# Kernel optimization log

Measured on AMD Instinct MI355X. Metric: run time of the kernel, lower is better.

The kernel has to match this reference:

```python
import jax, jax.numpy as jnp
import numpy as np

N_NODES = 50000
N_EDGES = 1600000
D_FEAT = 48


def setup_inputs() -> dict:
    key = jax.random.key(0)
    k1, k2, k3, k4, k5 = jax.random.split(key, 5)
    return {
        "x": jax.random.normal(k1, (N_EDGES, D_FEAT), dtype=jnp.float32),
        "switch": jax.random.uniform(k2, (N_EDGES,), dtype=jnp.float32),
        "edge_src": jax.random.randint(k3, (N_EDGES,), 0, N_NODES, dtype=jnp.int32),
        "edge_dst": jax.random.randint(k4, (N_EDGES,), 0, N_NODES, dtype=jnp.int32),
        "species": jax.random.randint(k5, (N_NODES,), 0, 100, dtype=jnp.int32),
    }


def reference(x, switch, edge_src, edge_dst, species):
    # nat = number of atoms, taken from species shape (static)
    nat = species.shape[0]
    # apply_switch: multiply per-edge switch into edge features [E, D] * [E, 1]
    xw = x * switch[:, None]
    # scatter-add edges to source atoms
    out = jax.ops.segment_sum(xw, edge_src, num_segments=nat)
    # antisymmetric: subtract scatter-add to destination atoms
    out = out - jax.ops.segment_sum(xw, edge_dst, num_segments=nat)
    return out  # [nat, D]
```

## Files before the change

### kernel.cpp

```cpp
#include <hip/hip_runtime.h>
#include <hip/hip_bf16.h>
#include <hip/hip_fp16.h>
#include <math.h>


#define D_FEAT 48
#define RNODES 64
#define RSHIFT 6
#define NB_MAX 1024
#define EPB 4096
#define SORT_CAP 8192

__global__ __launch_bounds__(256) void convert_kernel(
        const float4* __restrict__ x4, const float* __restrict__ sw,
        uint4* __restrict__ xwh, int G) {
    int g = blockIdx.x * 256 + threadIdx.x;
    if (g >= G) return;
    unsigned ug = (unsigned)g;
    int e = (int)(ug / 6u);
    float s = sw[e];
    const float4* p = x4 + (size_t)g * 2;
    float4 a = p[0], b = p[1];
    __half2 h0 = __floats2half2_rn(a.x * s, a.y * s);
    __half2 h1 = __floats2half2_rn(a.z * s, a.w * s);
    __half2 h2 = __floats2half2_rn(b.x * s, b.y * s);
    __half2 h3 = __floats2half2_rn(b.z * s, b.w * s);
    uint4 o;
    o.x = __builtin_bit_cast(unsigned int, h0);
    o.y = __builtin_bit_cast(unsigned int, h1);
    o.z = __builtin_bit_cast(unsigned int, h2);
    o.w = __builtin_bit_cast(unsigned int, h3);
    xwh[g] = o;
}

__global__ __launch_bounds__(256) void hist_kernel(
        const int* __restrict__ src, const int* __restrict__ dst,
        int* __restrict__ gcnt, int E, int NB) {
    __shared__ int lh[NB_MAX];
    for (int b = threadIdx.x; b < NB; b += 256) lh[b] = 0;
    __syncthreads();
    int t = threadIdx.x;
    int base = blockIdx.x * EPB;
    #pragma unroll
    for (int i = 0; i < EPB / 1024; ++i) {
        int e = base + i * 1024 + t * 4;
        if (e + 3 < E) {
            int4 s4 = *(const int4*)(src + e);
            int4 d4 = *(const int4*)(dst + e);
            atomicAdd(&lh[s4.x >> RSHIFT], 1);
            atomicAdd(&lh[s4.y >> RSHIFT], 1);
            atomicAdd(&lh[s4.z >> RSHIFT], 1);
            atomicAdd(&lh[s4.w >> RSHIFT], 1);
            atomicAdd(&lh[d4.x >> RSHIFT], 1);
            atomicAdd(&lh[d4.y >> RSHIFT], 1);
            atomicAdd(&lh[d4.z >> RSHIFT], 1);
            atomicAdd(&lh[d4.w >> RSHIFT], 1);
        } else {
            for (int j = 0; j < 4; ++j) {
                int ee = e + j;
                if (ee < E) {
                    atomicAdd(&lh[src[ee] >> RSHIFT], 1);
                    atomicAdd(&lh[dst[ee] >> RSHIFT], 1);
                }
            }
        }
    }
    __syncthreads();
    for (int b = threadIdx.x; b < NB; b += 256) {
        int c = lh[b];
        if (c) atomicAdd(&gcnt[b], c);
    }
}

__global__ __launch_bounds__(1024) void scan_kernel(
        const int* __restrict__ gcnt, int* __restrict__ goff,
        int* __restrict__ gcur, int* __restrict__ noff,
        int NB, int N, int total) {
    __shared__ int s[NB_MAX];
    int t = threadIdx.x;
    int v = (t < NB) ? gcnt[t] : 0;
    s[t] = v;
    __syncthreads();
    for (int d = 1; d < 1024; d <<= 1) {
        int a = (t >= d) ? s[t - d] : 0;
        __syncthreads();
        s[t] += a;
        __syncthreads();
    }
    if (t < NB) {
        int excl = s[t] - v;
        goff[t] = excl;
        gcur[t] = excl;
    }
    if (t == 0) {
        goff[NB] = total;
        noff[N] = total;
    }
}

__device__ __forceinline__ void bin_place(int e, int node, int side,
                                          int* lh, const int* lbase,
                                          int* __restrict__ items) {
    int b = node >> RSHIFT;
    int p = lbase[b] + atomicAdd(&lh[b], 1);
    items[p] = (e << 7) | (side << 6) | (node & (RNODES - 1));
}

__global__ __launch_bounds__(256) void bin_kernel(
        const int* __restrict__ src, const int* __restrict__ dst,
        int* __restrict__ gcur, int* __restrict__ items, int E, int NB) {
    __shared__ int lh[NB_MAX];
    __shared__ int lbase[NB_MAX];
    for (int b = threadIdx.x; b < NB; b += 256) lh[b] = 0;
    __syncthreads();
    int t = threadIdx.x;
    int base = blockIdx.x * EPB;
    #pragma unroll
    for (int i = 0; i < EPB / 1024; ++i) {
        int e = base + i * 1024 + t * 4;
        if (e + 3 < E) {
            int4 s4 = *(const int4*)(src + e);
            int4 d4 = *(const int4*)(dst + e);
            atomicAdd(&lh[s4.x >> RSHIFT], 1);
            atomicAdd(&lh[s4.y >> RSHIFT], 1);
            atomicAdd(&lh[s4.z >> RSHIFT], 1);
            atomicAdd(&lh[s4.w >> RSHIFT], 1);
            atomicAdd(&lh[d4.x >> RSHIFT], 1);
            atomicAdd(&lh[d4.y >> RSHIFT], 1);
            atomicAdd(&lh[d4.z >> RSHIFT], 1);
            atomicAdd(&lh[d4.w >> RSHIFT], 1);
        } else {
            for (int j = 0; j < 4; ++j) {
                int ee = e + j;
                if (ee < E) {
                    atomicAdd(&lh[src[ee] >> RSHIFT], 1);
                    atomicAdd(&lh[dst[ee] >> RSHIFT], 1);
                }
            }
        }
    }
    __syncthreads();
    for (int b = threadIdx.x; b < NB; b += 256) {
        int c = lh[b];
        lbase[b] = c ? atomicAdd(&gcur[b], c) : 0;
        lh[b] = 0;
    }
    __syncthreads();
    #pragma unroll
    for (int i = 0; i < EPB / 1024; ++i) {
        int e = base + i * 1024 + t * 4;
        if (e + 3 < E) {
            int4 s4 = *(const int4*)(src + e);
            int4 d4 = *(const int4*)(dst + e);
            bin_place(e + 0, s4.x, 0, lh, lbase, items);
            bin_place(e + 1, s4.y, 0, lh, lbase, items);
            bin_place(e + 2, s4.z, 0, lh, lbase, items);
            bin_place(e + 3, s4.w, 0, lh, lbase, items);
            bin_place(e + 0, d4.x, 1, lh, lbase, items);
            bin_place(e + 1, d4.y, 1, lh, lbase, items);
            bin_place(e + 2, d4.z, 1, lh, lbase, items);
            bin_place(e + 3, d4.w, 1, lh, lbase, items);
        } else {
            for (int j = 0; j < 4; ++j) {
                int ee = e + j;
                if (ee < E) {
                    bin_place(ee, src[ee], 0, lh, lbase, items);
                    bin_place(ee, dst[ee], 1, lh, lbase, items);
                }
            }
        }
    }
}

__global__ __launch_bounds__(256) void sort_kernel(
        int* __restrict__ items, const int* __restrict__ goff,
        int* __restrict__ noff, int N) {
    __shared__ int sitems[SORT_CAP];
    __shared__ int ccnt[RNODES];
    __shared__ int cbase[RNODES];
    int r = blockIdx.x;
    int lo = goff[r], hi = goff[r + 1];
    int cnt = hi - lo;
    int t = threadIdx.x;

    if (t < RNODES) ccnt[t] = 0;
    __syncthreads();
    #pragma unroll 4
    for (int i = t; i < cnt; i += 256) {
        int it = items[lo + i];
        sitems[i] = it;
        atomicAdd(&ccnt[it & (RNODES - 1)], 1);
    }
    __syncthreads();
    if (t < RNODES) {
        int c = ccnt[t];
        int v = c;
        #pragma unroll
        for (int d = 1; d < 64; d <<= 1) {
            int a = __shfl_up(v, d);
            if (t >= d) v += a;
        }
        int excl = v - c;
        cbase[t] = excl;
        int n = r * RNODES + t;
        if (n < N) noff[n] = lo + excl;
        ccnt[t] = 0;
    }
    __syncthreads();
    #pragma unroll 4
    for (int i = t; i < cnt; i += 256) {
        int it = sitems[i];
        int loc = it & (RNODES - 1);
        int p = cbase[loc] + atomicAdd(&ccnt[loc], 1);
        items[lo + p] = it;
    }
}

__global__ __launch_bounds__(256, 8) void gather_f16_kernel(
        const uint4* __restrict__ xwh, const int* __restrict__ noff,
        const int* __restrict__ items, float* __restrict__ out, int N) {
    int n = (blockIdx.x * blockDim.x + threadIdx.x) >> 6;
    int lane = threadIdx.x & 63;
    if (n >= N) return;

    int lo = noff[n], hi = noff[n + 1];
    int cnt = hi - lo;
    int grp = lane >> 3;
    int sub = lane & 7;

    float4 acc0 = make_float4(0.f, 0.f, 0.f, 0.f);
    float4 acc1 = make_float4(0.f, 0.f, 0.f, 0.f);

    for (int cb = 0; cb < cnt; cb += 64) {
        int chunk = items[lo + min(cb + lane, cnt - 1)];
        int rem = cnt - cb;
        #pragma unroll
        for (int k = 0; k < 8; ++k) {
            int idx = k * 8 + grp;
            int it = __shfl(chunk, idx);
            if (idx < rem && sub < 6) {
                uint4 q = xwh[(size_t)(it >> 7) * 6 + sub];
                unsigned m = (it & RNODES) ? 0x80008000u : 0u;
                float2 f0 = __half22float2(__builtin_bit_cast(__half2, q.x ^ m));
                float2 f1 = __half22float2(__builtin_bit_cast(__half2, q.y ^ m));
                float2 f2 = __half22float2(__builtin_bit_cast(__half2, q.z ^ m));
                float2 f3 = __half22float2(__builtin_bit_cast(__half2, q.w ^ m));
                acc0.x += f0.x; acc0.y += f0.y; acc0.z += f1.x; acc0.w += f1.y;
                acc1.x += f2.x; acc1.y += f2.y; acc1.z += f3.x; acc1.w += f3.y;
            }
        }
    }

    #pragma unroll
    for (int d = 32; d >= 8; d >>= 1) {
        acc0.x += __shfl_down(acc0.x, d);
        acc0.y += __shfl_down(acc0.y, d);
        acc0.z += __shfl_down(acc0.z, d);
        acc0.w += __shfl_down(acc0.w, d);
        acc1.x += __shfl_down(acc1.x, d);
        acc1.y += __shfl_down(acc1.y, d);
        acc1.z += __shfl_down(acc1.z, d);
        acc1.w += __shfl_down(acc1.w, d);
    }

    if (lane < 6) {
        float4* orow = (float4*)(out + (size_t)n * D_FEAT);
        orow[lane * 2 + 0] = acc0;
        orow[lane * 2 + 1] = acc1;
    }
}

__global__ __launch_bounds__(256, 4) void gather_kernel(
        const float4* __restrict__ x4, const float* __restrict__ sw,
        const int* __restrict__ noff, const int* __restrict__ items,
        float* __restrict__ out, int N) {
    int n = (blockIdx.x * blockDim.x + threadIdx.x) >> 6;
    int lane = threadIdx.x & 63;
    if (n >= N) return;

    int lo = noff[n], hi = noff[n + 1];
    int cnt = hi - lo;
    int grp = lane >> 4;
    int sub = lane & 15;

    float4 acc = make_float4(0.f, 0.f, 0.f, 0.f);

    for (int cb = 0; cb < cnt; cb += 64) {
        int chunk = items[lo + min(cb + lane, cnt - 1)];
        int rem = cnt - cb;
        #pragma unroll
        for (int k = 0; k < 16; ++k) {
            int idx = k * 4 + grp;
            int it = __shfl(chunk, idx);
            int e = it >> 7;
            float w = (idx < rem) ? sw[e] : 0.f;
            w = (it & RNODES) ? -w : w;
            if (sub < 12) {
                float4 v = x4[(size_t)e * 12 + sub];
                acc.x += w * v.x;
                acc.y += w * v.y;
                acc.z += w * v.z;
                acc.w += w * v.w;
            }
        }
    }

    acc.x += __shfl_down(acc.x, 32);
    acc.y += __shfl_down(acc.y, 32);
    acc.z += __shfl_down(acc.z, 32);
    acc.w += __shfl_down(acc.w, 32);
    acc.x += __shfl_down(acc.x, 16);
    acc.y += __shfl_down(acc.y, 16);
    acc.z += __shfl_down(acc.z, 16);
    acc.w += __shfl_down(acc.w, 16);

    if (lane < 12) {
        float4* orow = (float4*)(out + (size_t)n * D_FEAT);
        orow[lane] = acc;
    }
}

#define TPE 12
__global__ void atomic_fallback_kernel(const float4* __restrict__ x,
                                       const float* __restrict__ sw,
                                       const int* __restrict__ src,
                                       const int* __restrict__ dst,
                                       float* __restrict__ out, int n_edges) {
    int g = blockIdx.x * blockDim.x + threadIdx.x;
    int e = g / TPE;
    int q = g - e * TPE;
    if (e >= n_edges) return;
    float s = sw[e];
    float4 v = x[(size_t)e * TPE + q];
    v.x *= s; v.y *= s; v.z *= s; v.w *= s;
    int si = src[e], di = dst[e];
    float* po = out + (size_t)si * D_FEAT + q * 4;
    unsafeAtomicAdd(po + 0, v.x);
    unsafeAtomicAdd(po + 1, v.y);
    unsafeAtomicAdd(po + 2, v.z);
    unsafeAtomicAdd(po + 3, v.w);
    float* pd = out + (size_t)di * D_FEAT + q * 4;
    unsafeAtomicAdd(pd + 0, -v.x);
    unsafeAtomicAdd(pd + 1, -v.y);
    unsafeAtomicAdd(pd + 2, -v.z);
    unsafeAtomicAdd(pd + 3, -v.w);
}

extern "C" void kernel_launch(void* const* d_in, const int* in_sizes, int n_in,
                              void* d_out, int out_size, void* d_ws, size_t ws_size,
                              hipStream_t stream) {
    const float* x  = (const float*)d_in[0];
    const float* sw = (const float*)d_in[1];
    const int*   src = (const int*)d_in[2];
    const int*   dst = (const int*)d_in[3];
    float* out = (float*)d_out;

    int E = in_sizes[1];
    int N = in_sizes[4];
    int NB = (N + RNODES - 1) / RNODES;

    size_t xwh_bytes = (size_t)E * D_FEAT * 2;
    size_t need_int  = ((size_t)NB * 3 + 1 + (size_t)N + 1 + 2 * (size_t)E)
                       * sizeof(int);
    size_t need_f16  = xwh_bytes + need_int;

    int mean = (NB > 0) ? (int)((long long)2 * E / NB) : 0;
    bool bucket_risk = mean + 16 * (int)sqrtf((float)(mean > 0 ? mean : 1)) > SORT_CAP;

    if (NB > NB_MAX || ws_size < need_int || bucket_risk) {
        hipMemsetAsync(d_out, 0, (size_t)out_size * sizeof(float), stream);
        long long total = (long long)E * TPE;
        int grid = (int)((total + 255) / 256);
        atomic_fallback_kernel<<<grid, 256, 0, stream>>>(
            (const float4*)x, sw, src, dst, out, E);
        return;
    }

    bool use_f16 = (ws_size >= need_f16);
    char* base = (char*)d_ws;
    uint4* xwh = (uint4*)base;
    int* ints  = (int*)(use_f16 ? (base + xwh_bytes) : base);

    int* gcnt  = ints;
    int* goff  = gcnt + NB;
    int* gcur  = goff + NB + 1;
    int* noff  = gcur + NB;
    int* items = noff + N + 1;

    hipMemsetAsync(gcnt, 0, (size_t)NB * sizeof(int), stream);

    if (use_f16) {
        int G = E * (D_FEAT / 8);
        int cblk = (G + 255) / 256;
        convert_kernel<<<cblk, 256, 0, stream>>>((const float4*)x, sw, xwh, G);
    }

    int eblk = (E + EPB - 1) / EPB;
    hist_kernel<<<eblk, 256, 0, stream>>>(src, dst, gcnt, E, NB);
    scan_kernel<<<1, 1024, 0, stream>>>(gcnt, goff, gcur, noff, NB, N, 2 * E);
    bin_kernel<<<eblk, 256, 0, stream>>>(src, dst, gcur, items, E, NB);
    sort_kernel<<<NB, 256, 0, stream>>>(items, goff, noff, N);

    int gblk = (int)(((long long)N * 64 + 255) / 256);
    if (use_f16) {
        gather_f16_kernel<<<gblk, 256, 0, stream>>>(
            (const uint4*)xwh, noff, items, out, N);
    } else {
        gather_kernel<<<gblk, 256, 0, stream>>>(
            (const float4*)x, sw, noff, items, out, N);
    }
}
```

Baseline: 590.9 us.

## Fuse f16 conversion into hist/bin/sort kernels and pad rows to 128 bytes

Removes the standalone convert kernel and splits its work across extra blocks appended to the hist, bin and sort launches. The conversion then overlaps with those latency-bound, low-occupancy preprocessing kernels. Rows of the f16 edge buffer are padded from 6 to 8 uint4, so the gather uses all 8 lanes per edge and issues aligned 128-byte loads, at the cost of about a third more workspace and write traffic. Gather launch bounds are relaxed from 8 to 4 waves per EU.

```diff
diff --git a/kernel.cpp b/kernel.cpp
--- a/kernel.cpp
+++ b/kernel.cpp
@@ -10,33 +10,40 @@
 #define NB_MAX 1024
 #define EPB 4096
 #define SORT_CAP 8192
-
-__global__ __launch_bounds__(256) void convert_kernel(
+#define ROW_U4 8
+
+__device__ __forceinline__ void convert_one(int g, const float4* __restrict__ x4,
+                                            const float* __restrict__ sw,
+                                            uint4* __restrict__ xwh) {
+    int e = g >> 3, r = g & 7;
+    uint4 o = make_uint4(0u, 0u, 0u, 0u);
+    if (r < 6) {
+        float s = sw[e];
+        float4 a = x4[(size_t)e * 12 + r * 2];
+        float4 b = x4[(size_t)e * 12 + r * 2 + 1];
+        __half2 h0 = __floats2half2_rn(a.x * s, a.y * s);
+        __half2 h1 = __floats2half2_rn(a.z * s, a.w * s);
+        __half2 h2 = __floats2half2_rn(b.x * s, b.y * s);
+        __half2 h3 = __floats2half2_rn(b.z * s, b.w * s);
+        o.x = __builtin_bit_cast(unsigned int, h0);
+        o.y = __builtin_bit_cast(unsigned int, h1);
+        o.z = __builtin_bit_cast(unsigned int, h2);
+        o.w = __builtin_bit_cast(unsigned int, h3);
+    }
+    xwh[g] = o;
+}
+
+__global__ __launch_bounds__(256) void hist_cv_kernel(
+        const int* __restrict__ src, const int* __restrict__ dst,
+        int* __restrict__ gcnt, int E, int NB, int role_blocks,
         const float4* __restrict__ x4, const float* __restrict__ sw,
-        uint4* __restrict__ xwh, int G) {
-    int g = blockIdx.x * 256 + threadIdx.x;
-    if (g >= G) return;
-    unsigned ug = (unsigned)g;
-    int e = (int)(ug / 6u);
-    float s = sw[e];
-    const float4* p = x4 + (size_t)g * 2;
-    float4 a = p[0], b = p[1];
-    __half2 h0 = __floats2half2_rn(a.x * s, a.y * s);
-    __half2 h1 = __floats2half2_rn(a.z * s, a.w * s);
-    __half2 h2 = __floats2half2_rn(b.x * s, b.y * s);
-    __half2 h3 = __floats2half2_rn(b.z * s, b.w * s);
-    uint4 o;
-    o.x = __builtin_bit_cast(unsigned int, h0);
-    o.y = __builtin_bit_cast(unsigned int, h1);
-    o.z = __builtin_bit_cast(unsigned int, h2);
-    o.w = __builtin_bit_cast(unsigned int, h3);
-    xwh[g] = o;
-}
-
-__global__ __launch_bounds__(256) void hist_kernel(
-        const int* __restrict__ src, const int* __restrict__ dst,
-        int* __restrict__ gcnt, int E, int NB) {
+        uint4* __restrict__ xwh, int cv_g0, int cv_g1) {
     __shared__ int lh[NB_MAX];
+    if (blockIdx.x >= role_blocks) {
+        int g = cv_g0 + (blockIdx.x - role_blocks) * 256 + threadIdx.x;
+        if (g < cv_g1) convert_one(g, x4, sw, xwh);
+        return;
+    }
     for (int b = threadIdx.x; b < NB; b += 256) lh[b] = 0;
     __syncthreads();
     int t = threadIdx.x;
@@ -106,11 +113,19 @@
     items[p] = (e << 7) | (side << 6) | (node & (RNODES - 1));
 }
 
-__global__ __launch_bounds__(256) void bin_kernel(
+__global__ __launch_bounds__(256) void bin_cv_kernel(
         const int* __restrict__ src, const int* __restrict__ dst,
-        int* __restrict__ gcur, int* __restrict__ items, int E, int NB) {
+        int* __restrict__ gcur, int* __restrict__ items, int E, int NB,
+        int role_blocks,
+        const float4* __restrict__ x4, const float* __restrict__ sw,
+        uint4* __restrict__ xwh, int cv_g0, int cv_g1) {
     __shared__ int lh[NB_MAX];
     __shared__ int lbase[NB_MAX];
+    if (blockIdx.x >= role_blocks) {
+        int g = cv_g0 + (blockIdx.x - role_blocks) * 256 + threadIdx.x;
+        if (g < cv_g1) convert_one(g, x4, sw, xwh);
+        return;
+    }
     for (int b = threadIdx.x; b < NB; b += 256) lh[b] = 0;
     __syncthreads();
     int t = threadIdx.x;
@@ -172,12 +187,19 @@
     }
 }
 
-__global__ __launch_bounds__(256) void sort_kernel(
+__global__ __launch_bounds__(256) void sort_cv_kernel(
         int* __restrict__ items, const int* __restrict__ goff,
-        int* __restrict__ noff, int N) {
+        int* __restrict__ noff, int N, int role_blocks,
+        const float4* __restrict__ x4, const float* __restrict__ sw,
+        uint4* __restrict__ xwh, int cv_g0, int cv_g1) {
     __shared__ int sitems[SORT_CAP];
     __shared__ int ccnt[RNODES];
     __shared__ int cbase[RNODES];
+    if (blockIdx.x >= role_blocks) {
+        int g = cv_g0 + (blockIdx.x - role_blocks) * 256 + threadIdx.x;
+        if (g < cv_g1) convert_one(g, x4, sw, xwh);
+        return;
+    }
     int r = blockIdx.x;
     int lo = goff[r], hi = goff[r + 1];
     int cnt = hi - lo;
@@ -216,7 +238,7 @@
     }
 }
 
-__global__ __launch_bounds__(256, 8) void gather_f16_kernel(
+__global__ __launch_bounds__(256, 4) void gather_f16_kernel(
         const uint4* __restrict__ xwh, const int* __restrict__ noff,
         const int* __restrict__ items, float* __restrict__ out, int N) {
     int n = (blockIdx.x * blockDim.x + threadIdx.x) >> 6;
@@ -238,8 +260,8 @@
         for (int k = 0; k < 8; ++k) {
             int idx = k * 8 + grp;
             int it = __shfl(chunk, idx);
-            if (idx < rem && sub < 6) {
-                uint4 q = xwh[(size_t)(it >> 7) * 6 + sub];
+            if (idx < rem) {
+                uint4 q = xwh[(size_t)(unsigned)(it >> 7) * ROW_U4 + sub];
                 unsigned m = (it & RNODES) ? 0x80008000u : 0u;
                 float2 f0 = __half22float2(__builtin_bit_cast(__half2, q.x ^ m));
                 float2 f1 = __half22float2(__builtin_bit_cast(__half2, q.y ^ m));
@@ -359,7 +381,7 @@
     int N = in_sizes[4];
     int NB = (N + RNODES - 1) / RNODES;
 
-    size_t xwh_bytes = (size_t)E * D_FEAT * 2;
+    size_t xwh_bytes = (size_t)E * ROW_U4 * 16;
     size_t need_int  = ((size_t)NB * 3 + 1 + (size_t)N + 1 + 2 * (size_t)E)
                        * sizeof(int);
     size_t need_f16  = xwh_bytes + need_int;
@@ -389,17 +411,23 @@
 
     hipMemsetAsync(gcnt, 0, (size_t)NB * sizeof(int), stream);
 
-    if (use_f16) {
-        int G = E * (D_FEAT / 8);
-        int cblk = (G + 255) / 256;
-        convert_kernel<<<cblk, 256, 0, stream>>>((const float4*)x, sw, xwh, G);
-    }
+    int G = use_f16 ? E * 8 : 0;
+    int cvb = (G + 255) / 256;
+    int c1 = cvb / 3, c2 = cvb / 3, c3 = cvb - c1 - c2;
+    int g1 = c1 * 256, g2 = (c1 + c2) * 256;
 
     int eblk = (E + EPB - 1) / EPB;
-    hist_kernel<<<eblk, 256, 0, stream>>>(src, dst, gcnt, E, NB);
+
+    hist_cv_kernel<<<eblk + c1, 256, 0, stream>>>(
+        src, dst, gcnt, E, NB, eblk,
+        (const float4*)x, sw, xwh, 0, min(g1, G));
     scan_kernel<<<1, 1024, 0, stream>>>(gcnt, goff, gcur, noff, NB, N, 2 * E);
-    bin_kernel<<<eblk, 256, 0, stream>>>(src, dst, gcur, items, E, NB);
-    sort_kernel<<<NB, 256, 0, stream>>>(items, goff, noff, N);
+    bin_cv_kernel<<<eblk + c2, 256, 0, stream>>>(
+        src, dst, gcur, items, E, NB, eblk,
+        (const float4*)x, sw, xwh, g1, min(g2, G));
+    sort_cv_kernel<<<NB + c3, 256, 0, stream>>>(
+        items, goff, noff, N, NB,
+        (const float4*)x, sw, xwh, g2, G);
 
     int gblk = (int)(((long long)N * 64 + 255) / 256);
     if (use_f16) {
```

After: 561.9 us. -4.9%, faster.
